# Optimization experiments

Measured on AMD Instinct MI355X. Metric: run time of the kernel, lower is better.

## Reference

```python
import jax, jax.numpy as jnp
import numpy as np

NUM_CLASSES = 13
HIDDEN = 64
NUM_LAYERS = 2
NODE_FEAT = 1 + 4 + NUM_CLASSES  # 18
N_NODES = 100000
N_EDGES = 1600000


def _glorot(key, shape):
    fan_in, fan_out = shape[0], shape[1]
    lim = (6.0 / (fan_in + fan_out)) ** 0.5
    return jax.random.uniform(key, shape, jnp.float32, -lim, lim)


def setup_inputs() -> dict:
    key = jax.random.key(0)
    ks = jax.random.split(key, 32)
    H = HIDDEN
    inp = {
        "node_features": jax.random.normal(ks[0], (N_NODES, NODE_FEAT), jnp.float32),
        "edge_index": jax.random.randint(ks[1], (2, N_EDGES), 0, N_NODES, jnp.int32),
        "edge_weights": jax.random.uniform(ks[2], (N_EDGES,), jnp.float32),
        "embed_W": _glorot(ks[3], (NODE_FEAT, H)),
        "embed_b": jnp.zeros((H,), jnp.float32),
        # stacked per-layer params, leading dim = NUM_LAYERS
        "msg_W1": jnp.stack([_glorot(ks[4 + i], (2 * H, H)) for i in range(NUM_LAYERS)]),
        "msg_b1": jnp.zeros((NUM_LAYERS, H), jnp.float32),
        "msg_W2": jnp.stack([_glorot(ks[8 + i], (H, H)) for i in range(NUM_LAYERS)]),
        "msg_b2": jnp.zeros((NUM_LAYERS, H), jnp.float32),
        "att_W1": jnp.stack([_glorot(ks[12 + i], (2 * H, H // 2)) for i in range(NUM_LAYERS)]),
        "att_b1": jnp.zeros((NUM_LAYERS, H // 2), jnp.float32),
        "att_W2": jnp.stack([_glorot(ks[16 + i], (H // 2, 1)) for i in range(NUM_LAYERS)]),
        "att_b2": jnp.zeros((NUM_LAYERS, 1), jnp.float32),
        "upd_W1": jnp.stack([_glorot(ks[20 + i], (2 * H, H)) for i in range(NUM_LAYERS)]),
        "upd_b1": jnp.zeros((NUM_LAYERS, H), jnp.float32),
        "upd_W2": jnp.stack([_glorot(ks[24 + i], (H, H)) for i in range(NUM_LAYERS)]),
        "upd_b2": jnp.zeros((NUM_LAYERS, H), jnp.float32),
        "head_W": _glorot(ks[28], (H, 1)),
        "head_b": jnp.zeros((1,), jnp.float32),
    }
    return inp


def _mlp2(x, W1, b1, W2, b2):
    return jax.nn.relu(x @ W1 + b1) @ W2 + b2


def reference(node_features, edge_index, edge_weights,
              embed_W, embed_b,
              msg_W1, msg_b1, msg_W2, msg_b2,
              att_W1, att_b1, att_W2, att_b2,
              upd_W1, upd_b1, upd_W2, upd_b2,
              head_W, head_b):
    row, col = edge_index[0], edge_index[1]
    x = jax.nn.relu(node_features @ embed_W + embed_b)  # [N, H]
    num_nodes = x.shape[0]
    for l in range(NUM_LAYERS):
        cat = jnp.concatenate([x[row], x[col]], axis=-1)  # [E, 2H]
        messages = _mlp2(cat, msg_W1[l], msg_b1[l], msg_W2[l], msg_b2[l])  # [E, H]
        att = jax.nn.sigmoid(_mlp2(cat, att_W1[l], att_b1[l], att_W2[l], att_b2[l])[:, 0])  # [E]
        fw = edge_weights * att
        messages = messages * fw[:, None]
        aggregated = jax.ops.segment_sum(messages, col, num_segments=num_nodes)  # [N, H]
        norm = jax.ops.segment_sum(fw, col, num_segments=num_nodes)
        norm = jnp.clip(norm, 1e-6, None)
        aggregated = aggregated / norm[:, None]
        x_new = _mlp2(jnp.concatenate([x, aggregated], axis=-1),
                      upd_W1[l], upd_b1[l], upd_W2[l], upd_b2[l])
        x = jax.nn.relu(x_new + x)
    series_repr = jnp.max(x, axis=0)  # [H]
    binary_logit = (series_repr @ head_W + head_b)[0]
    return binary_logit
```

## Files before the change

### kernel.cpp

```cpp
#include <hip/hip_runtime.h>
#include <hip/hip_bf16.h>
#include <math.h>

#define H 64
#define F 18
#define NPW 2
#define NBKT 1024
#define EPB 8192

typedef _Float16 f16x8 __attribute__((ext_vector_type(8)));
typedef _Float16 f16x4 __attribute__((ext_vector_type(4)));
typedef _Float16 f16x2 __attribute__((ext_vector_type(2)));
typedef __fp16 h16x2 __attribute__((ext_vector_type(2)));
typedef float f32x4 __attribute__((ext_vector_type(4)));

__global__ __launch_bounds__(256) void prep_update_kernel(
    const float* __restrict__ mW2, const float* __restrict__ mb2,
    const float* __restrict__ uW1,
    float* __restrict__ M2U, float* __restrict__ mbu)
{
    int t = blockIdx.x * 256 + threadIdx.x;
    if (t >= 2 * 64 * 64) return;
    int l = t >> 12, r = t & 4095;
    int i = r >> 6, j = r & 63;
    const float* W2 = mW2 + (size_t)l * 4096;
    const float* U1b = uW1 + (size_t)l * 8192 + 4096;
    float s = 0.f;
    for (int k = 0; k < 64; ++k) s += W2[i * 64 + k] * U1b[k * 64 + j];
    M2U[t] = s;
    if (i == 0) {
        float sb = 0.f;
        const float* b2 = mb2 + (size_t)l * 64;
        for (int k = 0; k < 64; ++k) sb += b2[k] * U1b[k * 64 + j];
        mbu[l * 64 + j] = sb;
    }
}

__global__ __launch_bounds__(256) void packfrag_all_kernel(
    const float* __restrict__ mW1, const float* __restrict__ aW1,
    const float* __restrict__ uW1, const float* __restrict__ M2U,
    const float* __restrict__ uW2, const float* __restrict__ eW,
    f16x8* __restrict__ uvB, f16x8* __restrict__ updB,
    f16x8* __restrict__ embB)
{
    int t = blockIdx.x * 256 + threadIdx.x;
    if (t >= 6400) return;
    int lane = t & 63;
    int frag = t >> 6;
    int quad = lane >> 4, l15 = lane & 15;
    if (frag < 48) {
        int l = frag / 24, rem = frag % 24;
        int side = rem / 12, q = rem % 12;
        int nt = q >> 1, kk = q & 1;
        int col = nt * 16 + l15;
        f16x8 v;
#pragma unroll
        for (int j = 0; j < 8; ++j) {
            int k = side * 64 + kk * 32 + quad * 8 + j;
            float w = (col < 64) ? mW1[(size_t)l * 8192 + k * 64 + col]
                                 : aW1[(size_t)l * 4096 + k * 32 + (col - 64)];
            v[j] = (_Float16)w;
        }
        uvB[(size_t)frag * 64 + lane] = v;
    } else if (frag < 96) {
        int f2 = frag - 48;
        int l = f2 / 24, f = f2 % 24;
        int g = f >> 3, ff = f & 7;
        int nt = ff >> 1, kk = ff & 1;
        const float* src;
        if (g == 0)      src = uW1 + (size_t)l * 8192;
        else if (g == 1) src = M2U + (size_t)l * 4096;
        else             src = uW2 + (size_t)l * 4096;
        f16x8 v;
#pragma unroll
        for (int j = 0; j < 8; ++j) {
            int k = kk * 32 + quad * 8 + j;
            v[j] = (_Float16)src[k * 64 + nt * 16 + l15];
        }
        updB[(size_t)f2 * 64 + lane] = v;
    } else {
        int nt = frag - 96;
        f16x8 v;
#pragma unroll
        for (int j = 0; j < 8; ++j) {
            int k = quad * 8 + j;
            v[j] = (k < F) ? (_Float16)eW[k * 64 + nt * 16 + l15] : (_Float16)0;
        }
        embB[(size_t)nt * 64 + lane] = v;
    }
}

__global__ __launch_bounds__(256) void scan1_kernel(
    const int* __restrict__ deg, int* __restrict__ part,
    int* __restrict__ bsum, int N)
{
    __shared__ int lds[256];
    int t = threadIdx.x;
    int base = blockIdx.x * 1024 + t * 4;
    int v[4];
#pragma unroll
    for (int s = 0; s < 4; ++s) v[s] = (base + s < N) ? deg[base + s] : 0;
    int sum = v[0] + v[1] + v[2] + v[3];
    lds[t] = sum;
    __syncthreads();
    for (int off = 1; off < 256; off <<= 1) {
        int xv = (t >= off) ? lds[t - off] : 0;
        __syncthreads();
        lds[t] += xv;
        __syncthreads();
    }
    int excl = lds[t] - sum;
    if (t == 255) bsum[blockIdx.x] = lds[255];
    int p = excl;
#pragma unroll
    for (int s = 0; s < 4; ++s) {
        if (base + s < N) part[base + s] = p;
        p += v[s];
    }
}

__global__ __launch_bounds__(256) void scan2_kernel(int* __restrict__ bsum, int nb)
{
    __shared__ int lds[256];
    int t = threadIdx.x;
    int v = (t < nb) ? bsum[t] : 0;
    lds[t] = v;
    __syncthreads();
    for (int off = 1; off < 256; off <<= 1) {
        int xv = (t >= off) ? lds[t - off] : 0;
        __syncthreads();
        lds[t] += xv;
        __syncthreads();
    }
    if (t < nb) bsum[t] = lds[t] - v;
}

__global__ __launch_bounds__(256) void count_bucket_kernel(
    const int* __restrict__ col, int* __restrict__ cnt,
    unsigned int* __restrict__ serp, int E, int NB, int NBK, int BS)
{
    __shared__ int lc[NBKT];
    int t = threadIdx.x;
    if (blockIdx.x == 0 && t < 64) serp[t] = 0;
    for (int i = t; i < NBK; i += 256) lc[i] = 0;
    __syncthreads();
    for (int s = 0; s < EPB / 256; ++s) {
        int e = blockIdx.x * EPB + s * 256 + t;
        if (e < E) atomicAdd(lc + (unsigned)col[e] / (unsigned)BS, 1);
    }
    __syncthreads();
    for (int i = t; i < NBK; i += 256)
        cnt[(size_t)i * NB + blockIdx.x] = lc[i];
}

__global__ __launch_bounds__(256) void place_kernel(
    const int* __restrict__ row, const int* __restrict__ col,
    const float* __restrict__ ew, const int* __restrict__ off,
    const int* __restrict__ bsum,
    int2* __restrict__ edata, int E, int NB, int NBK, int BS)
{
    __shared__ int lc[NBKT];
    int t = threadIdx.x;
    for (int i = t; i < NBK; i += 256) lc[i] = 0;
    __syncthreads();
    for (int s = 0; s < EPB / 256; ++s) {
        int e = blockIdx.x * EPB + s * 256 + t;
        if (e < E) {
            int cv = col[e];
            int c = (unsigned)cv / (unsigned)BS;
            int lcol = cv - c * BS;
            int r = atomicAdd(lc + c, 1);
            int idx = c * NB + blockIdx.x;
            int pos = off[idx] + bsum[idx >> 10] + r;
            edata[pos] = make_int2(row[e] | (lcol << 20), __float_as_int(ew[e]));
        }
    }
}

__global__ __launch_bounds__(256) void bucket_sort_kernel(
    int2* __restrict__ edata, const int* __restrict__ off,
    const int* __restrict__ bsum,
    int* __restrict__ deg, int* __restrict__ startp,
    int NB, int BS, int N, int E, int NBK)
{
    __shared__ int hist[256];
    __shared__ int psum[256];
    int b = blockIdx.x;
    int t = threadIdx.x;
    int i0 = b * NB;
    int base = off[i0] + bsum[i0 >> 10];
    int end = E;
    if (b + 1 < NBK) {
        int i1 = (b + 1) * NB;
        end = off[i1] + bsum[i1 >> 10];
    }
    int cnt = end - base;
    int nlo = b * BS;

    hist[t] = 0;
    __syncthreads();

    int2 regs[8];
    int lnode[8];
#pragma unroll
    for (int ii = 0; ii < 8; ++ii) {
        int i = t + ii * 256;
        if (i < cnt) {
            regs[ii] = edata[base + i];
            lnode[ii] = ((unsigned)regs[ii].x) >> 20;
            atomicAdd(hist + lnode[ii], 1);
        }
    }
    __syncthreads();

    int cv = hist[t];
    psum[t] = cv;
    __syncthreads();
    for (int o = 1; o < 256; o <<= 1) {
        int xv = (t >= o) ? psum[t - o] : 0;
        __syncthreads();
        psum[t] += xv;
        __syncthreads();
    }
    int excl = psum[t] - cv;
    int ng = nlo + t;
    if (t < BS && ng < N) {
        deg[ng] = cv;
        startp[ng] = base + excl;
    }
    hist[t] = excl;
    __syncthreads();

#pragma unroll
    for (int ii = 0; ii < 8; ++ii) {
        int i = t + ii * 256;
        if (i < cnt) {
            int pos = atomicAdd(hist + lnode[ii], 1);
            edata[base + pos] = make_int2(regs[ii].x & 0xFFFFF, regs[ii].y);
        }
    }
}

__global__ __launch_bounds__(64, 2) void embed_uv_kernel(
    const float* __restrict__ nf, const f16x8* __restrict__ embB,
    const float* __restrict__ eb,
    const f16x8* __restrict__ uvB0,
    const float* __restrict__ mb1, const float* __restrict__ ab1,
    _Float16* __restrict__ xh, _Float16* __restrict__ UV, int N)
{
    __shared__ __align__(16) _Float16 hlds[16 * 80];
    int lane = threadIdx.x;
    int wid = blockIdx.x;
    int quad = lane >> 4, l15 = lane & 15;
    int nbase = wid * 64;
    if (nbase >= N) return;

    f16x8 Be[4];
#pragma unroll
    for (int i = 0; i < 4; ++i) Be[i] = embB[i * 64 + lane];
    f16x8 B[24];
#pragma unroll
    for (int i = 0; i < 24; ++i) B[i] = uvB0[i * 64 + lane];
    float bve[4];
#pragma unroll
    for (int nt = 0; nt < 4; ++nt) bve[nt] = eb[nt * 16 + l15];
    float bvn[12];
#pragma unroll
    for (int q = 0; q < 12; ++q) {
        int sd = q / 6, nt2 = q % 6;
        int col = nt2 * 16 + l15;
        bvn[q] = sd ? 0.f : (col < 64 ? mb1[col] : ab1[col - 64]);
    }

    for (int mt = 0; mt < 4; ++mt) {
        int na = nbase + mt * 16 + l15;
        if (na >= N) na = N - 1;
        f16x8 Ax;
#pragma unroll
        for (int j = 0; j < 8; ++j) {
            int k = quad * 8 + j;
            Ax[j] = (k < F) ? (_Float16)nf[(size_t)na * F + k] : (_Float16)0;
        }

        f32x4 C[4];
#pragma unroll
        for (int nt = 0; nt < 4; ++nt) {
            f32x4 cc = {bve[nt], bve[nt], bve[nt], bve[nt]};
            cc = __builtin_amdgcn_mfma_f32_16x16x32_f16(Ax, Be[nt], cc, 0, 0, 0);
            C[nt] = cc;
        }

        int noder = nbase + mt * 16 + quad * 4;
        float xn[4][4];
#pragma unroll
        for (int r = 0; r < 4; ++r) {
            int ng = noder + r;
#pragma unroll
            for (int nt = 0; nt < 4; ++nt) {
                float v = fmaxf(C[nt][r], 0.f);
                xn[nt][r] = v;
                if (ng < N) xh[(size_t)ng * H + nt * 16 + l15] = (_Float16)v;
            }
        }

#pragma unroll
        for (int nt = 0; nt < 4; ++nt)
#pragma unroll
            for (int r = 0; r < 4; ++r)
                hlds[(quad * 4 + r) * 80 + nt * 16 + l15] = (_Float16)xn[nt][r];
        __asm__ __volatile__("s_waitcnt lgkmcnt(0)" ::: "memory");
        f16x8 A2[2];
        A2[0] = *(const f16x8*)&hlds[l15 * 80 + quad * 8];
        A2[1] = *(const f16x8*)&hlds[l15 * 80 + 32 + quad * 8];
        __asm__ __volatile__("s_waitcnt lgkmcnt(0)" ::: "memory");

#pragma unroll
        for (int q = 0; q < 12; ++q) {
            int sd = q / 6, nt2 = q % 6;
            f32x4 cc = {bvn[q], bvn[q], bvn[q], bvn[q]};
            cc = __builtin_amdgcn_mfma_f32_16x16x32_f16(A2[0], B[sd * 12 + nt2 * 2], cc, 0, 0, 0);
            cc = __builtin_amdgcn_mfma_f32_16x16x32_f16(A2[1], B[sd * 12 + nt2 * 2 + 1], cc, 0, 0, 0);
#pragma unroll
            for (int r = 0; r < 4; ++r) {
                int n = noder + r;
                if (n < N)
                    UV[(size_t)n * 192 + sd * 96 + nt2 * 16 + l15] = (_Float16)cc[r];
            }
        }
    }
}

__global__ __launch_bounds__(256) void edge_gather_kernel(
    const _Float16* __restrict__ UV,
    const int2* __restrict__ edata,
    const int* __restrict__ startp, const int* __restrict__ deg,
    const float* __restrict__ aW2, const float* __restrict__ ab2,
    _Float16* __restrict__ aggN, float* __restrict__ snorm, int N)
{
    int wid = (blockIdx.x * 256 + threadIdx.x) >> 6;
    int lane = threadIdx.x & 63;
    int g = lane >> 3, s = lane & 7;
    int n0 = wid * NPW;
    if (n0 >= N) return;
    int n1 = n0 + NPW; if (n1 > N) n1 = N;

    float aw2v[4];
#pragma unroll
    for (int j = 0; j < 4; ++j) aw2v[j] = aW2[s * 4 + j];
#if __has_builtin(__builtin_amdgcn_fdot2)
    h16x2 aw01, aw23;
    aw01[0] = (__fp16)aw2v[0]; aw01[1] = (__fp16)aw2v[1];
    aw23[0] = (__fp16)aw2v[2]; aw23[1] = (__fp16)aw2v[3];
#endif
    float ab2v = ab2[0];
    const f16x2 zer = {(_Float16)0, (_Float16)0};

    typedef union { f16x8 v; f16x2 p[4]; } u8p;
    typedef union { f16x4 v; f16x2 p[2]; h16x2 h[2]; } u4p;

    for (int n = n0; n < n1; ++n) {
        int e0 = startp[n];
        int d = deg[n];
        int iters = (d + 7) >> 3;
        const _Float16* vrow = UV + (size_t)n * 192 + 96;
        u8p vm; vm.v = *(const f16x8*)(vrow + s * 8);
        u4p va; va.v = *(const f16x4*)(vrow + 64 + s * 4);

        float acc[8];
#pragma unroll
        for (int j = 0; j < 8; ++j) acc[j] = 0.f;
        float rfw = 0.f;

        if (iters > 0) {
            int2 ed0, ed1 = {0, 0}, ed2 = {0, 0};
            u8p um0;
            u4p ua0;
            {
                int ei = g;
                ed0 = edata[e0 + (ei < d ? ei : 0)];
                const _Float16* ur = UV + (size_t)ed0.x * 192;
                um0.v = *(const f16x8*)(ur + s * 8);
                ua0.v = *(const f16x4*)(ur + 64 + s * 4);
            }
            if (iters > 1) {
                int ei = 8 + g;
                ed1 = edata[e0 + (ei < d ? ei : 0)];
            }
            for (int it = 0; it < iters; ++it) {
                u8p umn = um0;
                u4p uan = ua0;
                if (it + 1 < iters) {
                    const _Float16* ur = UV + (size_t)ed1.x * 192;
                    umn.v = *(const f16x8*)(ur + s * 8);
                    uan.v = *(const f16x4*)(ur + 64 + s * 4);
                }
                if (it + 2 < iters) {
                    int ei = (it + 2) * 8 + g;
                    ed2 = edata[e0 + (ei < d ? ei : 0)];
                }

                int ei = it * 8 + g;
                float ew = (ei < d) ? __int_as_float(ed0.y) : 0.f;
                f16x2 za0 = __builtin_elementwise_max(ua0.p[0] + va.p[0], zer);
                f16x2 za1 = __builtin_elementwise_max(ua0.p[1] + va.p[1], zer);
#if __has_builtin(__builtin_amdgcn_fdot2)
                h16x2 hz0, hz1;
                __builtin_memcpy(&hz0, &za0, 4);
                __builtin_memcpy(&hz1, &za1, 4);
                float pp = __builtin_amdgcn_fdot2(
                    hz0, aw01,
                    __builtin_amdgcn_fdot2(hz1, aw23, 0.f, false), false);
#else
                float pp = (float)za0[0] * aw2v[0] + (float)za0[1] * aw2v[1]
                         + (float)za1[0] * aw2v[2] + (float)za1[1] * aw2v[3];
#endif
                pp += __int_as_float(__builtin_amdgcn_update_dpp(
                    0, __float_as_int(pp), 0xB1, 0xF, 0xF, true));
                pp += __int_as_float(__builtin_amdgcn_update_dpp(
                    0, __float_as_int(pp), 0x4E, 0xF, 0xF, true));
                pp += __shfl_xor(pp, 4);
                float fw = ew * __builtin_amdgcn_rcpf(1.f + __expf(-(pp + ab2v)));
#pragma unroll
                for (int j = 0; j < 4; ++j) {
                    f16x2 z = __builtin_elementwise_max(um0.p[j] + vm.p[j], zer);
                    acc[2 * j]     += (float)z[0] * fw;
                    acc[2 * j + 1] += (float)z[1] * fw;
                }
                rfw += fw;

                ed0 = ed1; ed1 = ed2; um0 = umn; ua0 = uan;
            }
        }

#pragma unroll
        for (int o = 8; o <= 32; o <<= 1) {
#pragma unroll
            for (int j = 0; j < 8; ++j) acc[j] += __shfl_xor(acc[j], o);
            rfw += __shfl_xor(rfw, o);
        }
        float inv = 1.f / fmaxf(rfw, 1e-6f);
        if (g == 0) {
            union { _Float16 h[8]; uint4 v; } O;
#pragma unroll
            for (int j = 0; j < 8; ++j) O.h[j] = (_Float16)(acc[j] * inv);
            *(uint4*)(aggN + (size_t)n * H + s * 8) = O.v;
        }
        if (lane == 0) snorm[n] = rfw * inv;
    }
}

__global__ __launch_bounds__(64, 2) void update_mfma_kernel(
    _Float16* __restrict__ xh, const _Float16* __restrict__ agg,
    const float* __restrict__ snorm,
    const f16x8* __restrict__ Bfrag,
    const float* __restrict__ mbu,
    const float* __restrict__ ub1, const float* __restrict__ ub2,
    const f16x8* __restrict__ uvBn,
    const float* __restrict__ mb1n, const float* __restrict__ ab1n,
    _Float16* __restrict__ UV,
    unsigned int* __restrict__ serp,
    int N, int doMax)
{
    __shared__ __align__(16) _Float16 hlds[16 * 80];
    int lane = threadIdx.x;
    int wid = blockIdx.x;
    int quad = lane >> 4, l15 = lane & 15;
    int nbase = wid * 64;
    if (nbase >= N) return;

    f16x8 Bu[8], Bm[8], Bw[8];
#pragma unroll
    for (int i = 0; i < 8; ++i) {
        Bu[i] = Bfrag[i * 64 + lane];
        Bm[i] = Bfrag[(8 + i) * 64 + lane];
        Bw[i] = Bfrag[(16 + i) * 64 + lane];
    }
    float mbuv[4], b1v[4], b2v[4];
#pragma unroll
    for (int nt = 0; nt < 4; ++nt) {
        mbuv[nt] = mbu[nt * 16 + l15];
        b1v[nt] = ub1[nt * 16 + l15];
        b2v[nt] = ub2[nt * 16 + l15];
    }
    float bvn[12];
    if (uvBn) {
#pragma unroll
        for (int q = 0; q < 12; ++q) {
            int sd = q / 6, nt2 = q % 6;
            int col = nt2 * 16 + l15;
            bvn[q] = sd ? 0.f : (col < 64 ? mb1n[col] : ab1n[col - 64]);
        }
    }
    float lmax[4] = {0.f, 0.f, 0.f, 0.f};

    for (int mt = 0; mt < 4; ++mt) {
        int na = nbase + mt * 16 + l15;
        if (na >= N) na = N - 1;
        const f16x8* xrow = (const f16x8*)(xh + (size_t)na * H);
        f16x8 Ax[2];
        Ax[0] = xrow[quad];
        Ax[1] = xrow[4 + quad];
        const f16x8* arow = (const f16x8*)(agg + (size_t)na * H);
        f16x8 Aa[2];
        Aa[0] = arow[quad];
        Aa[1] = arow[4 + quad];

        f32x4 Cx[4], Ca[4];
#pragma unroll
        for (int nt = 0; nt < 4; ++nt) {
            f32x4 cx = {0.f, 0.f, 0.f, 0.f}, ca = {0.f, 0.f, 0.f, 0.f};
#pragma unroll
            for (int kk = 0; kk < 2; ++kk) {
                cx = __builtin_amdgcn_mfma_f32_16x16x32_f16(Ax[kk], Bu[nt * 2 + kk], cx, 0, 0, 0);
                ca = __builtin_amdgcn_mfma_f32_16x16x32_f16(Aa[kk], Bm[nt * 2 + kk], ca, 0, 0, 0);
            }
            Cx[nt] = cx; Ca[nt] = ca;
        }

        int noder = nbase + mt * 16 + quad * 4;
        float sn_r[4];
#pragma unroll
        for (int r = 0; r < 4; ++r) {
            int ng = noder + r; if (ng >= N) ng = N - 1;
            sn_r[r] = snorm[ng];
        }

#pragma unroll
        for (int nt = 0; nt < 4; ++nt) {
#pragma unroll
            for (int r = 0; r < 4; ++r) {
                float hv = fmaxf(Cx[nt][r] + Ca[nt][r]
                                 + sn_r[r] * mbuv[nt] + b1v[nt], 0.f);
                hlds[(quad * 4 + r) * 80 + nt * 16 + l15] = (_Float16)hv;
            }
        }
        __asm__ __volatile__("s_waitcnt lgkmcnt(0)" ::: "memory");
        f16x8 Ah[2];
        Ah[0] = *(const f16x8*)&hlds[l15 * 80 + quad * 8];
        Ah[1] = *(const f16x8*)&hlds[l15 * 80 + 32 + quad * 8];
        __asm__ __volatile__("s_waitcnt lgkmcnt(0)" ::: "memory");

        f32x4 C2[4];
#pragma unroll
        for (int nt = 0; nt < 4; ++nt) {
            f32x4 cc = {0.f, 0.f, 0.f, 0.f};
#pragma unroll
            for (int kk = 0; kk < 2; ++kk)
                cc = __builtin_amdgcn_mfma_f32_16x16x32_f16(Ah[kk], Bw[nt * 2 + kk], cc, 0, 0, 0);
            C2[nt] = cc;
        }

        float xn[4][4];
#pragma unroll
        for (int r = 0; r < 4; ++r) {
            int ng = noder + r;
            if (ng < N) {
#pragma unroll
                for (int nt = 0; nt < 4; ++nt) {
                    size_t idx = (size_t)ng * H + nt * 16 + l15;
                    float xo = (float)xh[idx];
                    float v = fmaxf(C2[nt][r] + b2v[nt] + xo, 0.f);
                    xn[nt][r] = v;
                    xh[idx] = (_Float16)v;
                }
            } else {
#pragma unroll
                for (int nt = 0; nt < 4; ++nt) xn[nt][r] = 0.f;
            }
        }
        if (doMax) {
#pragma unroll
            for (int nt = 0; nt < 4; ++nt)
#pragma unroll
                for (int r = 0; r < 4; ++r) lmax[nt] = fmaxf(lmax[nt], xn[nt][r]);
        }

        if (uvBn) {
#pragma unroll
            for (int nt = 0; nt < 4; ++nt)
#pragma unroll
                for (int r = 0; r < 4; ++r)
                    hlds[(quad * 4 + r) * 80 + nt * 16 + l15] = (_Float16)xn[nt][r];
            __asm__ __volatile__("s_waitcnt lgkmcnt(0)" ::: "memory");
            f16x8 A2[2];
            A2[0] = *(const f16x8*)&hlds[l15 * 80 + quad * 8];
            A2[1] = *(const f16x8*)&hlds[l15 * 80 + 32 + quad * 8];
            __asm__ __volatile__("s_waitcnt lgkmcnt(0)" ::: "memory");

#pragma unroll
            for (int q = 0; q < 12; ++q) {
                int sd = q / 6, nt2 = q % 6;
                f16x8 Ba = uvBn[(sd * 12 + nt2 * 2) * 64 + lane];
                f16x8 Bb = uvBn[(sd * 12 + nt2 * 2 + 1) * 64 + lane];
                f32x4 cc = {bvn[q], bvn[q], bvn[q], bvn[q]};
                cc = __builtin_amdgcn_mfma_f32_16x16x32_f16(A2[0], Ba, cc, 0, 0, 0);
                cc = __builtin_amdgcn_mfma_f32_16x16x32_f16(A2[1], Bb, cc, 0, 0, 0);
#pragma unroll
                for (int r = 0; r < 4; ++r) {
                    int n = noder + r;
                    if (n < N)
                        UV[(size_t)n * 192 + sd * 96 + nt2 * 16 + l15] = (_Float16)cc[r];
                }
            }
        }
    }

    if (doMax) {
#pragma unroll
        for (int nt = 0; nt < 4; ++nt) {
            float m = lmax[nt];
            m = fmaxf(m, __shfl_xor(m, 16));
            m = fmaxf(m, __shfl_xor(m, 32));
            if (quad == 0) atomicMax(serp + nt * 16 + l15, __float_as_uint(m));
        }
    }
}

__global__ void head_kernel(const unsigned int* __restrict__ serp,
                            const float* __restrict__ hW,
                            const float* __restrict__ hb,
                            float* __restrict__ out)
{
    int j = threadIdx.x;
    float v = __uint_as_float(serp[j]) * hW[j];
#pragma unroll
    for (int off = 32; off > 0; off >>= 1) v += __shfl_down(v, off);
    if (j == 0) out[0] = v + hb[0];
}

extern "C" void kernel_launch(void* const* d_in, const int* in_sizes, int n_in,
                              void* d_out, int out_size, void* d_ws, size_t ws_size,
                              hipStream_t stream)
{
    const float* nf  = (const float*)d_in[0];
    const int*   ei  = (const int*)d_in[1];
    const float* ew  = (const float*)d_in[2];
    const float* eW  = (const float*)d_in[3];
    const float* eb_ = (const float*)d_in[4];
    const float* mW1 = (const float*)d_in[5];
    const float* mb1 = (const float*)d_in[6];
    const float* mW2 = (const float*)d_in[7];
    const float* mb2 = (const float*)d_in[8];
    const float* aW1 = (const float*)d_in[9];
    const float* ab1 = (const float*)d_in[10];
    const float* aW2 = (const float*)d_in[11];
    const float* ab2 = (const float*)d_in[12];
    const float* uW1 = (const float*)d_in[13];
    const float* ub1 = (const float*)d_in[14];
    const float* uW2 = (const float*)d_in[15];
    const float* ub2 = (const float*)d_in[16];
    const float* hW  = (const float*)d_in[17];
    const float* hb  = (const float*)d_in[18];

    int N = in_sizes[0] / F;
    int E = in_sizes[2];
    const int* row = ei;
    const int* col = ei + E;

    size_t Nr = ((size_t)N + 3) & ~(size_t)3;
    size_t Er = ((size_t)E + 3) & ~(size_t)3;

    int BS  = (N + NBKT - 1) / NBKT;
    int NBK = (N + BS - 1) / BS;
    int NB  = (E + EPB - 1) / EPB;
    size_t M  = (size_t)NBK * NB;
    size_t Mr = (M + 3) & ~(size_t)3;

    _Float16* xh   = (_Float16*)d_ws;
    _Float16* aggN = xh + Nr * 64;
    float* snorm   = (float*)(aggN + Nr * 64);
    unsigned int* serp = (unsigned int*)(snorm + Nr);
    int* deg       = (int*)(serp + 64);
    int* startp    = deg + Nr;
    int* bsum      = startp + Nr;
    float* M2U     = (float*)(bsum + 256);
    float* mbu     = M2U + 8192;
    f16x8* updB    = (f16x8*)(mbu + 128);
    f16x8* uvB     = updB + 3072;
    f16x8* embB    = uvB + 3072;
    _Float16* UV   = (_Float16*)(embB + 256);
    int* cnt       = (int*)(UV + Nr * 192);
    int* off       = cnt + Mr;
    int2* edata    = (int2*)(off + Mr);

    int nbA = (int)((M + 1023) / 1024);

    count_bucket_kernel<<<NB, 256, 0, stream>>>(col, cnt, serp, E, NB, NBK, BS);
    scan1_kernel<<<nbA, 256, 0, stream>>>(cnt, off, bsum, (int)M);
    scan2_kernel<<<1, 256, 0, stream>>>(bsum, nbA);
    place_kernel<<<NB, 256, 0, stream>>>(row, col, ew, off, bsum, edata, E, NB, NBK, BS);
    bucket_sort_kernel<<<NBK, 256, 0, stream>>>(edata, off, bsum, deg, startp,
                                                NB, BS, N, E, NBK);

    prep_update_kernel<<<32, 256, 0, stream>>>(mW2, mb2, uW1, M2U, mbu);
    packfrag_all_kernel<<<25, 256, 0, stream>>>(mW1, aW1, uW1, M2U, uW2, eW,
                                                uvB, updB, embB);

    int nwaves_n = (N + 63) / 64;
    int nb_eg = (N + NPW * 4 - 1) / (NPW * 4);

    embed_uv_kernel<<<nwaves_n, 64, 0, stream>>>(
        nf, embB, eb_, uvB, mb1, ab1, xh, UV, N);
    edge_gather_kernel<<<nb_eg, 256, 0, stream>>>(
        UV, edata, startp, deg, aW2, ab2, aggN, snorm, N);
    update_mfma_kernel<<<nwaves_n, 64, 0, stream>>>(
        xh, aggN, snorm, updB, mbu, ub1, ub2,
        uvB + 24 * 64, mb1 + H, ab1 + (H / 2), UV, nullptr, N, 0);
    edge_gather_kernel<<<nb_eg, 256, 0, stream>>>(
        UV, edata, startp, deg, aW2 + (H / 2), ab2 + 1, aggN, snorm, N);
    update_mfma_kernel<<<nwaves_n, 64, 0, stream>>>(
        xh, aggN, snorm, updB + 24 * 64, mbu + 64, ub1 + H, ub2 + H,
        nullptr, nullptr, nullptr, nullptr, serp, N, 1);

    head_kernel<<<1, 64, 0, stream>>>(serp, hW, hb, (float*)d_out);
}
```

Before: 368.5 us.

## Fuse graph-build and weight-prep kernels into one cooperative kernel with grid syncs

Seven preprocessing launches (bucket count, two scans, place, bucket sort, weight product, fragment packing) are merged into a single cooperative kernel of 512 blocks separated by grid.sync barriers. The edge partition changes from fixed 8192-edge chunks to 512 equal chunks, and the weight preparation work rides on otherwise idle blocks within phases. This removes per-launch overhead and gaps between small kernels, at the cost of grid-wide barriers, fewer blocks for the bucket-sort phase (a loop over buckets), and the requirement that all 512 blocks be co-resident.

```diff
diff --git a/kernel.cpp b/kernel.cpp
--- a/kernel.cpp
+++ b/kernel.cpp
@@ -1,12 +1,15 @@
 #include <hip/hip_runtime.h>
 #include <hip/hip_bf16.h>
+#include <hip/hip_cooperative_groups.h>
 #include <math.h>
+
+namespace cg = cooperative_groups;
 
 #define H 64
 #define F 18
 #define NPW 2
 #define NBKT 1024
-#define EPB 8192
+#define CNB 512
 
 typedef _Float16 f16x8 __attribute__((ext_vector_type(8)));
 typedef _Float16 f16x4 __attribute__((ext_vector_type(4)));
@@ -14,230 +17,219 @@
 typedef __fp16 h16x2 __attribute__((ext_vector_type(2)));
 typedef float f32x4 __attribute__((ext_vector_type(4)));
 
-__global__ __launch_bounds__(256) void prep_update_kernel(
+__global__ __launch_bounds__(256, 2) void coop_build_kernel(
+    const int* __restrict__ row, const int* __restrict__ col,
+    const float* __restrict__ ew,
     const float* __restrict__ mW2, const float* __restrict__ mb2,
-    const float* __restrict__ uW1,
-    float* __restrict__ M2U, float* __restrict__ mbu)
+    const float* __restrict__ uW1, const float* __restrict__ mW1,
+    const float* __restrict__ aW1, const float* __restrict__ uW2,
+    const float* __restrict__ eW,
+    float* __restrict__ M2U, float* __restrict__ mbu,
+    f16x8* __restrict__ uvB, f16x8* __restrict__ updB,
+    f16x8* __restrict__ embB,
+    int* __restrict__ cnt, int* __restrict__ off, int* __restrict__ bsum,
+    unsigned int* __restrict__ serp,
+    int2* __restrict__ edata, int* __restrict__ deg, int* __restrict__ startp,
+    int E, int N, int NBK, int BS, int EPB2)
 {
-    int t = blockIdx.x * 256 + threadIdx.x;
-    if (t >= 2 * 64 * 64) return;
-    int l = t >> 12, r = t & 4095;
-    int i = r >> 6, j = r & 63;
-    const float* W2 = mW2 + (size_t)l * 4096;
-    const float* U1b = uW1 + (size_t)l * 8192 + 4096;
-    float s = 0.f;
-    for (int k = 0; k < 64; ++k) s += W2[i * 64 + k] * U1b[k * 64 + j];
-    M2U[t] = s;
-    if (i == 0) {
-        float sb = 0.f;
-        const float* b2 = mb2 + (size_t)l * 64;
-        for (int k = 0; k < 64; ++k) sb += b2[k] * U1b[k * 64 + j];
-        mbu[l * 64 + j] = sb;
-    }
-}
-
-__global__ __launch_bounds__(256) void packfrag_all_kernel(
-    const float* __restrict__ mW1, const float* __restrict__ aW1,
-    const float* __restrict__ uW1, const float* __restrict__ M2U,
-    const float* __restrict__ uW2, const float* __restrict__ eW,
-    f16x8* __restrict__ uvB, f16x8* __restrict__ updB,
-    f16x8* __restrict__ embB)
-{
-    int t = blockIdx.x * 256 + threadIdx.x;
-    if (t >= 6400) return;
-    int lane = t & 63;
-    int frag = t >> 6;
-    int quad = lane >> 4, l15 = lane & 15;
-    if (frag < 48) {
-        int l = frag / 24, rem = frag % 24;
-        int side = rem / 12, q = rem % 12;
-        int nt = q >> 1, kk = q & 1;
-        int col = nt * 16 + l15;
-        f16x8 v;
-#pragma unroll
-        for (int j = 0; j < 8; ++j) {
-            int k = side * 64 + kk * 32 + quad * 8 + j;
-            float w = (col < 64) ? mW1[(size_t)l * 8192 + k * 64 + col]
-                                 : aW1[(size_t)l * 4096 + k * 32 + (col - 64)];
-            v[j] = (_Float16)w;
-        }
-        uvB[(size_t)frag * 64 + lane] = v;
-    } else if (frag < 96) {
-        int f2 = frag - 48;
-        int l = f2 / 24, f = f2 % 24;
-        int g = f >> 3, ff = f & 7;
-        int nt = ff >> 1, kk = ff & 1;
-        const float* src;
-        if (g == 0)      src = uW1 + (size_t)l * 8192;
-        else if (g == 1) src = M2U + (size_t)l * 4096;
-        else             src = uW2 + (size_t)l * 4096;
-        f16x8 v;
-#pragma unroll
-        for (int j = 0; j < 8; ++j) {
-            int k = kk * 32 + quad * 8 + j;
-            v[j] = (_Float16)src[k * 64 + nt * 16 + l15];
-        }
-        updB[(size_t)f2 * 64 + lane] = v;
-    } else {
-        int nt = frag - 96;
-        f16x8 v;
-#pragma unroll
-        for (int j = 0; j < 8; ++j) {
-            int k = quad * 8 + j;
-            v[j] = (k < F) ? (_Float16)eW[k * 64 + nt * 16 + l15] : (_Float16)0;
-        }
-        embB[(size_t)nt * 64 + lane] = v;
-    }
-}
-
-__global__ __launch_bounds__(256) void scan1_kernel(
-    const int* __restrict__ deg, int* __restrict__ part,
-    int* __restrict__ bsum, int N)
-{
-    __shared__ int lds[256];
+    cg::grid_group grid = cg::this_grid();
+    __shared__ int shm[NBKT];
+    int b = blockIdx.x;
     int t = threadIdx.x;
-    int base = blockIdx.x * 1024 + t * 4;
-    int v[4];
-#pragma unroll
-    for (int s = 0; s < 4; ++s) v[s] = (base + s < N) ? deg[base + s] : 0;
-    int sum = v[0] + v[1] + v[2] + v[3];
-    lds[t] = sum;
+    int nsteps = (EPB2 + 255) / 256;
+    int estart = b * EPB2;
+    int eend = estart + EPB2; if (eend > E) eend = E;
+    int M = NBK * CNB;
+    int nbScan = (M + 1023) / 1024;
+
+    if (b == 0 && t < 64) serp[t] = 0;
+    for (int i = t; i < NBK; i += 256) shm[i] = 0;
     __syncthreads();
-    for (int off = 1; off < 256; off <<= 1) {
-        int xv = (t >= off) ? lds[t - off] : 0;
-        __syncthreads();
-        lds[t] += xv;
-        __syncthreads();
-    }
-    int excl = lds[t] - sum;
-    if (t == 255) bsum[blockIdx.x] = lds[255];
-    int p = excl;
-#pragma unroll
-    for (int s = 0; s < 4; ++s) {
-        if (base + s < N) part[base + s] = p;
-        p += v[s];
-    }
-}
-
-__global__ __launch_bounds__(256) void scan2_kernel(int* __restrict__ bsum, int nb)
-{
-    __shared__ int lds[256];
-    int t = threadIdx.x;
-    int v = (t < nb) ? bsum[t] : 0;
-    lds[t] = v;
-    __syncthreads();
-    for (int off = 1; off < 256; off <<= 1) {
-        int xv = (t >= off) ? lds[t - off] : 0;
-        __syncthreads();
-        lds[t] += xv;
-        __syncthreads();
-    }
-    if (t < nb) bsum[t] = lds[t] - v;
-}
-
-__global__ __launch_bounds__(256) void count_bucket_kernel(
-    const int* __restrict__ col, int* __restrict__ cnt,
-    unsigned int* __restrict__ serp, int E, int NB, int NBK, int BS)
-{
-    __shared__ int lc[NBKT];
-    int t = threadIdx.x;
-    if (blockIdx.x == 0 && t < 64) serp[t] = 0;
-    for (int i = t; i < NBK; i += 256) lc[i] = 0;
-    __syncthreads();
-    for (int s = 0; s < EPB / 256; ++s) {
-        int e = blockIdx.x * EPB + s * 256 + t;
-        if (e < E) atomicAdd(lc + (unsigned)col[e] / (unsigned)BS, 1);
+    for (int s = 0; s < nsteps; ++s) {
+        int e = estart + s * 256 + t;
+        if (e < eend) atomicAdd(shm + (unsigned)col[e] / (unsigned)BS, 1);
     }
     __syncthreads();
     for (int i = t; i < NBK; i += 256)
-        cnt[(size_t)i * NB + blockIdx.x] = lc[i];
-}
-
-__global__ __launch_bounds__(256) void place_kernel(
-    const int* __restrict__ row, const int* __restrict__ col,
-    const float* __restrict__ ew, const int* __restrict__ off,
-    const int* __restrict__ bsum,
-    int2* __restrict__ edata, int E, int NB, int NBK, int BS)
-{
-    __shared__ int lc[NBKT];
-    int t = threadIdx.x;
-    for (int i = t; i < NBK; i += 256) lc[i] = 0;
+        cnt[(size_t)i * CNB + b] = shm[i];
+    if (b >= CNB - 32) {
+        int tp = (b - (CNB - 32)) * 256 + t;
+        int l = tp >> 12, r = tp & 4095;
+        int i = r >> 6, j = r & 63;
+        const float* W2 = mW2 + (size_t)l * 4096;
+        const float* U1b = uW1 + (size_t)l * 8192 + 4096;
+        float s = 0.f;
+        for (int k = 0; k < 64; ++k) s += W2[i * 64 + k] * U1b[k * 64 + j];
+        M2U[tp] = s;
+        if (i == 0) {
+            float sb = 0.f;
+            const float* b2 = mb2 + (size_t)l * 64;
+            for (int k = 0; k < 64; ++k) sb += b2[k] * U1b[k * 64 + j];
+            mbu[l * 64 + j] = sb;
+        }
+    }
+    grid.sync();
+
+    if (b < nbScan) {
+        int base = b * 1024 + t * 4;
+        int v[4];
+#pragma unroll
+        for (int s = 0; s < 4; ++s) v[s] = (base + s < M) ? cnt[base + s] : 0;
+        int sum = v[0] + v[1] + v[2] + v[3];
+        shm[t] = sum;
+        __syncthreads();
+        for (int o = 1; o < 256; o <<= 1) {
+            int xv = (t >= o) ? shm[t - o] : 0;
+            __syncthreads();
+            shm[t] += xv;
+            __syncthreads();
+        }
+        int excl = shm[t] - sum;
+        if (t == 255) bsum[b] = shm[255];
+        int p = excl;
+#pragma unroll
+        for (int s = 0; s < 4; ++s) {
+            if (base + s < M) off[base + s] = p;
+            p += v[s];
+        }
+    }
+    grid.sync();
+
+    if (b == 0) {
+        int v0 = (2 * t < nbScan) ? bsum[2 * t] : 0;
+        int v1 = (2 * t + 1 < nbScan) ? bsum[2 * t + 1] : 0;
+        int sum = v0 + v1;
+        shm[t] = sum;
+        __syncthreads();
+        for (int o = 1; o < 256; o <<= 1) {
+            int xv = (t >= o) ? shm[t - o] : 0;
+            __syncthreads();
+            shm[t] += xv;
+            __syncthreads();
+        }
+        int excl = shm[t] - sum;
+        if (2 * t < nbScan) bsum[2 * t] = excl;
+        if (2 * t + 1 < nbScan) bsum[2 * t + 1] = excl + v0;
+    } else if (b <= 25) {
+        int tp = (b - 1) * 256 + t;
+        if (tp < 6400) {
+            int lane = tp & 63;
+            int frag = tp >> 6;
+            int quad = lane >> 4, l15 = lane & 15;
+            if (frag < 48) {
+                int l = frag / 24, rem = frag % 24;
+                int side = rem / 12, q = rem % 12;
+                int nt = q >> 1, kk = q & 1;
+                int colx = nt * 16 + l15;
+                f16x8 v;
+#pragma unroll
+                for (int j = 0; j < 8; ++j) {
+                    int k = side * 64 + kk * 32 + quad * 8 + j;
+                    float w = (colx < 64) ? mW1[(size_t)l * 8192 + k * 64 + colx]
+                                          : aW1[(size_t)l * 4096 + k * 32 + (colx - 64)];
+                    v[j] = (_Float16)w;
+                }
+                uvB[(size_t)frag * 64 + lane] = v;
+            } else if (frag < 96) {
+                int f2 = frag - 48;
+                int l = f2 / 24, f = f2 % 24;
+                int g = f >> 3, ff = f & 7;
+                int nt = ff >> 1, kk = ff & 1;
+                const float* src;
+                if (g == 0)      src = uW1 + (size_t)l * 8192;
+                else if (g == 1) src = M2U + (size_t)l * 4096;
+                else             src = uW2 + (size_t)l * 4096;
+                f16x8 v;
+#pragma unroll
+                for (int j = 0; j < 8; ++j) {
+                    int k = kk * 32 + quad * 8 + j;
+                    v[j] = (_Float16)src[k * 64 + nt * 16 + l15];
+                }
+                updB[(size_t)f2 * 64 + lane] = v;
+            } else {
+                int nt = frag - 96;
+                f16x8 v;
+#pragma unroll
+                for (int j = 0; j < 8; ++j) {
+                    int k = quad * 8 + j;
+                    v[j] = (k < F) ? (_Float16)eW[k * 64 + nt * 16 + l15]
+                                   : (_Float16)0;
+                }
+                embB[(size_t)nt * 64 + lane] = v;
+            }
+        }
+    }
+    grid.sync();
+
+    for (int i = t; i < NBK; i += 256) shm[i] = 0;
     __syncthreads();
-    for (int s = 0; s < EPB / 256; ++s) {
-        int e = blockIdx.x * EPB + s * 256 + t;
-        if (e < E) {
+    for (int s = 0; s < nsteps; ++s) {
+        int e = estart + s * 256 + t;
+        if (e < eend) {
             int cv = col[e];
             int c = (unsigned)cv / (unsigned)BS;
             int lcol = cv - c * BS;
-            int r = atomicAdd(lc + c, 1);
-            int idx = c * NB + blockIdx.x;
+            int r = atomicAdd(shm + c, 1);
+            int idx = c * CNB + b;
             int pos = off[idx] + bsum[idx >> 10] + r;
             edata[pos] = make_int2(row[e] | (lcol << 20), __float_as_int(ew[e]));
         }
     }
-}
-
-__global__ __launch_bounds__(256) void bucket_sort_kernel(
-    int2* __restrict__ edata, const int* __restrict__ off,
-    const int* __restrict__ bsum,
-    int* __restrict__ deg, int* __restrict__ startp,
-    int NB, int BS, int N, int E, int NBK)
-{
-    __shared__ int hist[256];
-    __shared__ int psum[256];
-    int b = blockIdx.x;
-    int t = threadIdx.x;
-    int i0 = b * NB;
-    int base = off[i0] + bsum[i0 >> 10];
-    int end = E;
-    if (b + 1 < NBK) {
-        int i1 = (b + 1) * NB;
-        end = off[i1] + bsum[i1 >> 10];
-    }
-    int cnt = end - base;
-    int nlo = b * BS;
-
-    hist[t] = 0;
-    __syncthreads();
-
-    int2 regs[8];
-    int lnode[8];
-#pragma unroll
-    for (int ii = 0; ii < 8; ++ii) {
-        int i = t + ii * 256;
-        if (i < cnt) {
-            regs[ii] = edata[base + i];
-            lnode[ii] = ((unsigned)regs[ii].x) >> 20;
-            atomicAdd(hist + lnode[ii], 1);
-        }
-    }
-    __syncthreads();
-
-    int cv = hist[t];
-    psum[t] = cv;
-    __syncthreads();
-    for (int o = 1; o < 256; o <<= 1) {
-        int xv = (t >= o) ? psum[t - o] : 0;
+    grid.sync();
+
+    int* hist = shm;
+    int* psum = shm + 256;
+    for (int bkt = b; bkt < NBK; bkt += CNB) {
+        int i0 = bkt * CNB;
+        int base = off[i0] + bsum[i0 >> 10];
+        int end = E;
+        if (bkt + 1 < NBK) {
+            int i1 = (bkt + 1) * CNB;
+            end = off[i1] + bsum[i1 >> 10];
+        }
+        int cntE = end - base;
+        int nlo = bkt * BS;
+
+        hist[t] = 0;
         __syncthreads();
-        psum[t] += xv;
+        int2 regs[8];
+        int lnode[8];
+#pragma unroll
+        for (int ii = 0; ii < 8; ++ii) {
+            int i = t + ii * 256;
+            if (i < cntE) {
+                regs[ii] = edata[base + i];
+                lnode[ii] = ((unsigned)regs[ii].x) >> 20;
+                atomicAdd(hist + lnode[ii], 1);
+            }
+        }
         __syncthreads();
-    }
-    int excl = psum[t] - cv;
-    int ng = nlo + t;
-    if (t < BS && ng < N) {
-        deg[ng] = cv;
-        startp[ng] = base + excl;
-    }
-    hist[t] = excl;
-    __syncthreads();
-
-#pragma unroll
-    for (int ii = 0; ii < 8; ++ii) {
-        int i = t + ii * 256;
-        if (i < cnt) {
-            int pos = atomicAdd(hist + lnode[ii], 1);
-            edata[base + pos] = make_int2(regs[ii].x & 0xFFFFF, regs[ii].y);
-        }
+        int cv = hist[t];
+        psum[t] = cv;
+        __syncthreads();
+        for (int o = 1; o < 256; o <<= 1) {
+            int xv = (t >= o) ? psum[t - o] : 0;
+            __syncthreads();
+            psum[t] += xv;
+            __syncthreads();
+        }
+        int excl = psum[t] - cv;
+        int ng = nlo + t;
+        if (t < BS && ng < N) {
+            deg[ng] = cv;
+            startp[ng] = base + excl;
+        }
+        hist[t] = excl;
+        __syncthreads();
+#pragma unroll
+        for (int ii = 0; ii < 8; ++ii) {
+            int i = t + ii * 256;
+            if (i < cntE) {
+                int pos = atomicAdd(hist + lnode[ii], 1);
+                edata[base + pos] = make_int2(regs[ii].x & 0xFFFFF, regs[ii].y);
+            }
+        }
+        __syncthreads();
     }
 }
 
@@ -662,8 +654,8 @@
 
     int BS  = (N + NBKT - 1) / NBKT;
     int NBK = (N + BS - 1) / BS;
-    int NB  = (E + EPB - 1) / EPB;
-    size_t M  = (size_t)NBK * NB;
+    int EPB2 = (E + CNB - 1) / CNB;
+    size_t M  = (size_t)NBK * CNB;
     size_t Mr = (M + 3) & ~(size_t)3;
 
     _Float16* xh   = (_Float16*)d_ws;
@@ -673,7 +665,7 @@
     int* deg       = (int*)(serp + 64);
     int* startp    = deg + Nr;
     int* bsum      = startp + Nr;
-    float* M2U     = (float*)(bsum + 256);
+    float* M2U     = (float*)(bsum + 512);
     float* mbu     = M2U + 8192;
     f16x8* updB    = (f16x8*)(mbu + 128);
     f16x8* uvB     = updB + 3072;
@@ -683,18 +675,16 @@
     int* off       = cnt + Mr;
     int2* edata    = (int2*)(off + Mr);
 
-    int nbA = (int)((M + 1023) / 1024);
-
-    count_bucket_kernel<<<NB, 256, 0, stream>>>(col, cnt, serp, E, NB, NBK, BS);
-    scan1_kernel<<<nbA, 256, 0, stream>>>(cnt, off, bsum, (int)M);
-    scan2_kernel<<<1, 256, 0, stream>>>(bsum, nbA);
-    place_kernel<<<NB, 256, 0, stream>>>(row, col, ew, off, bsum, edata, E, NB, NBK, BS);
-    bucket_sort_kernel<<<NBK, 256, 0, stream>>>(edata, off, bsum, deg, startp,
-                                                NB, BS, N, E, NBK);
-
-    prep_update_kernel<<<32, 256, 0, stream>>>(mW2, mb2, uW1, M2U, mbu);
-    packfrag_all_kernel<<<25, 256, 0, stream>>>(mW1, aW1, uW1, M2U, uW2, eW,
-                                                uvB, updB, embB);
+    void* cargs[] = {
+        (void*)&row, (void*)&col, (void*)&ew,
+        (void*)&mW2, (void*)&mb2, (void*)&uW1, (void*)&mW1,
+        (void*)&aW1, (void*)&uW2, (void*)&eW,
+        (void*)&M2U, (void*)&mbu, (void*)&uvB, (void*)&updB, (void*)&embB,
+        (void*)&cnt, (void*)&off, (void*)&bsum, (void*)&serp,
+        (void*)&edata, (void*)&deg, (void*)&startp,
+        (void*)&E, (void*)&N, (void*)&NBK, (void*)&BS, (void*)&EPB2 };
+    (void)hipLaunchCooperativeKernel((void*)coop_build_kernel,
+                                     dim3(CNB), dim3(256), cargs, 0, stream);
 
     int nwaves_n = (N + 63) / 64;
     int nb_eg = (N + NPW * 4 - 1) / (NPW * 4);
```

After: 641.7 us. 1.74x slower.
